# Kernel tuning notes

Hardware: AMD Instinct MI355X
Metric: run time of the kernel (lower is better)

## Reference

```python
import jax, jax.numpy as jnp
import numpy as np

NN_SIZE = 10  # k nearest neighbors (includes the point itself)
EPS = 1e-8


def batch_normals(points_nchw, nn_size):
    # points_nchw: (B, 3, N)
    x = jnp.transpose(points_nchw, (0, 2, 1))  # (B, N, 3)
    sq = jnp.sum(x * x, axis=-1)  # (B, N)
    # pairwise squared distances (B, N, N)
    d2 = sq[:, :, None] + sq[:, None, :] - 2.0 * jnp.einsum('bnd,bmd->bnm', x, x)
    _, idx = jax.lax.top_k(-d2, nn_size)  # (B, N, k) nearest-neighbor indices
    # irregular gather of neighborhoods: (B, N, k, 3)
    neigh = jax.vmap(lambda p, i: p[i])(x, idx)
    centered = neigh - jnp.mean(neigh, axis=2, keepdims=True)
    # local 3x3 covariance per point
    cov = jnp.einsum('bnki,bnkj->bnij', centered, centered) / nn_size
    _, vecs = jnp.linalg.eigh(cov)  # eigenvalues ascending
    normals = vecs[..., 0]  # eigenvector of smallest eigenvalue, (B, N, 3), unit norm
    return jnp.transpose(normals, (0, 2, 1))  # (B, 3, N)


def setup_inputs() -> dict:
    key = jax.random.key(0)
    k1, k2 = jax.random.split(key)
    pred = jax.random.normal(k1, (8, 3, 4096), dtype=jnp.float32)
    gt = jax.random.normal(k2, (8, 3, 4096), dtype=jnp.float32)
    return {"pred": pred, "gt": gt}


def reference(pred, gt):
    pn = batch_normals(pred, NN_SIZE)  # (B, 3, N)
    gn = batch_normals(gt, NN_SIZE)    # (B, 3, N)
    # cosine similarity along the channel (coordinate) dim
    dot = jnp.sum(pn * gn, axis=1)
    denom = jnp.sqrt(jnp.sum(pn * pn, axis=1)) * jnp.sqrt(jnp.sum(gn * gn, axis=1))
    cos = dot / jnp.maximum(denom, EPS)
    return jnp.mean(1.0 - jnp.abs(cos))
```

## Files before the change

### kernel.cpp

```cpp
#include <hip/hip_runtime.h>
#include <float.h>
#include <math.h>

#define BATCH 8
#define NPTS 4096
#define KNN 10
#define BN (BATCH * NPTS)
#define QPB 64
#define SEGS 4
#define HALF (NPTS / 2)
#define SEGC (HALF / SEGS)

__device__ inline float med3f(float x, float a, float b) {
    return __builtin_amdgcn_fmed3f(x, a, b);
}

__device__ inline void smallest_eigvec(float a00, float a01, float a02,
                                       float a11, float a12, float a22,
                                       float& vx, float& vy, float& vz) {
    float p1 = a01 * a01 + a02 * a02 + a12 * a12;
    float q = (a00 + a11 + a22) * (1.0f / 3.0f);
    float b00 = a00 - q, b11 = a11 - q, b22 = a22 - q;
    float p2 = b00 * b00 + b11 * b11 + b22 * b22 + 2.0f * p1;
    float p = sqrtf(p2 * (1.0f / 6.0f));
    if (p < 1e-20f) { vx = 1.0f; vy = 0.0f; vz = 0.0f; return; }
    float ip = 1.0f / p;
    float c00 = b00 * ip, c01 = a01 * ip, c02 = a02 * ip;
    float c11 = b11 * ip, c12 = a12 * ip, c22 = b22 * ip;
    float detB = c00 * (c11 * c22 - c12 * c12)
               - c01 * (c01 * c22 - c12 * c02)
               + c02 * (c01 * c12 - c11 * c02);
    float r = 0.5f * detB;
    r = fminf(1.0f, fmaxf(-1.0f, r));
    float phi = acosf(r) * (1.0f / 3.0f);
    float lmin = q + 2.0f * p * cosf(phi + 2.0943951023931953f);

    float m00 = a00 - lmin, m11 = a11 - lmin, m22 = a22 - lmin;
    float r0x = m00, r0y = a01, r0z = a02;
    float r1x = a01, r1y = m11, r1z = a12;
    float r2x = a02, r2y = a12, r2z = m22;
    float c0x = r0y * r1z - r0z * r1y, c0y = r0z * r1x - r0x * r1z, c0z = r0x * r1y - r0y * r1x;
    float c1x = r0y * r2z - r0z * r2y, c1y = r0z * r2x - r0x * r2z, c1z = r0x * r2y - r0y * r2x;
    float c2x = r1y * r2z - r1z * r2y, c2y = r1z * r2x - r1x * r2z, c2z = r1x * r2y - r1y * r2x;
    float n0 = c0x * c0x + c0y * c0y + c0z * c0z;
    float n1 = c1x * c1x + c1y * c1y + c1z * c1z;
    float n2 = c2x * c2x + c2y * c2y + c2z * c2z;
    float bx = c0x, by = c0y, bz = c0z, bnm = n0;
    if (n1 > bnm) { bx = c1x; by = c1y; bz = c1z; bnm = n1; }
    if (n2 > bnm) { bx = c2x; by = c2y; bz = c2z; bnm = n2; }
    if (bnm < 1e-30f) { vx = 1.0f; vy = 0.0f; vz = 0.0f; return; }
    float inv = rsqrtf(bnm);
    vx = bx * inv; vy = by * inv; vz = bz * inv;
}

__global__ __launch_bounds__(256, 4) void knn_normals_kernel(
    const float* __restrict__ pred, const float* __restrict__ gt,
    float* __restrict__ normals ) {
    __shared__ float4 pts[HALF];
    __shared__ float keybuf[3 * QPB * KNN];

    const int b = blockIdx.y;
    const int cloud = blockIdx.z;
    const float* __restrict__ base = (cloud == 0 ? pred : gt) + b * 3 * NPTS;
    const int tid = threadIdx.x;
    const int q = tid & (QPB - 1);
    const int seg = tid >> 6;
    const int pt = blockIdx.x * QPB + q;

    const float mex = base[pt];
    const float mey = base[NPTS + pt];
    const float mez = base[2 * NPTS + pt];
    const float nmx = -2.0f * mex, nmy = -2.0f * mey, nmz = -2.0f * mez;
    const float smw = mex * mex + mey * mey + mez * mez;

    float k[KNN];
#pragma unroll
    for (int j = 0; j < KNN; ++j) k[j] = FLT_MAX;

    for (int pass = 0; pass < 2; ++pass) {
        const int pb = pass * HALF;
        for (int i = tid; i < HALF; i += 256) {
            float x = base[pb + i];
            float y = base[NPTS + pb + i];
            float z = base[2 * NPTS + pb + i];
            pts[i] = make_float4(x, y, z, x * x + y * y + z * z);
        }
        __syncthreads();

        const int s0 = seg * SEGC;
        const unsigned gbase = (unsigned)(pb + s0);
#pragma unroll 8
        for (int c = 0; c < SEGC; ++c) {
            float4 p = pts[s0 + c];
            float d = fmaf(p.z, nmz, fmaf(p.y, nmy, fmaf(p.x, nmx, p.w + smw)));
            d = fmaxf(d, 1e-30f);
            float key = __uint_as_float((__float_as_uint(d) & 0xFFFFF000u) | (gbase + c));
#pragma unroll
            for (int j = KNN - 1; j >= 1; --j) k[j] = med3f(key, k[j - 1], k[j]);
            k[0] = fminf(key, k[0]);
        }
        __syncthreads();
    }

    if (seg != 0) {
#pragma unroll
        for (int j = 0; j < KNN; ++j) keybuf[((seg - 1) * QPB + q) * KNN + j] = k[j];
    }
    __syncthreads();

    if (seg == 0) {
        for (int s = 0; s < 3; ++s) {
#pragma unroll
            for (int jj = 0; jj < KNN; ++jj) {
                float key = keybuf[(s * QPB + q) * KNN + jj];
#pragma unroll
                for (int j = KNN - 1; j >= 1; --j) k[j] = med3f(key, k[j - 1], k[j]);
                k[0] = fminf(key, k[0]);
            }
        }

        float nx[KNN], ny[KNN], nz[KNN];
        float mx = 0.f, my = 0.f, mz = 0.f;
#pragma unroll
        for (int j = 0; j < KNN; ++j) {
            int idx = (int)(__float_as_uint(k[j]) & 0xFFFu);
            nx[j] = base[idx]; ny[j] = base[NPTS + idx]; nz[j] = base[2 * NPTS + idx];
            mx += nx[j]; my += ny[j]; mz += nz[j];
        }
        mx *= (1.0f / KNN); my *= (1.0f / KNN); mz *= (1.0f / KNN);

        float cxx = 0.f, cxy = 0.f, cxz = 0.f, cyy = 0.f, cyz = 0.f, czz = 0.f;
#pragma unroll
        for (int j = 0; j < KNN; ++j) {
            float dx = nx[j] - mx, dy = ny[j] - my, dz = nz[j] - mz;
            cxx += dx * dx; cxy += dx * dy; cxz += dx * dz;
            cyy += dy * dy; cyz += dy * dz; czz += dz * dz;
        }
        cxx *= (1.0f / KNN); cxy *= (1.0f / KNN); cxz *= (1.0f / KNN);
        cyy *= (1.0f / KNN); cyz *= (1.0f / KNN); czz *= (1.0f / KNN);

        float vx, vy, vz;
        smallest_eigvec(cxx, cxy, cxz, cyy, cyz, czz, vx, vy, vz);

        float* outp = normals + cloud * 3 * BN;
        const int oidx = b * NPTS + pt;
        outp[oidx] = vx;
        outp[BN + oidx] = vy;
        outp[2 * BN + oidx] = vz;
    }
}

__global__ void zero_out_kernel(float* __restrict__ out) {
    if (threadIdx.x == 0) out[0] = 0.0f;
}

__global__ __launch_bounds__(256) void loss_kernel(const float* __restrict__ normals,
                                                   float* __restrict__ out) {
    __shared__ float red[256];
    const float* pn = normals;
    const float* gn = normals + 3 * BN;
    float acc = 0.f;
    for (int i = blockIdx.x * 256 + threadIdx.x; i < BN; i += 64 * 256) {
        float px = pn[i], py = pn[BN + i], pz = pn[2 * BN + i];
        float gx = gn[i], gy = gn[BN + i], gz = gn[2 * BN + i];
        float dot = px * gx + py * gy + pz * gz;
        float npn = sqrtf(px * px + py * py + pz * pz);
        float ngn = sqrtf(gx * gx + gy * gy + gz * gz);
        float denom = fmaxf(npn * ngn, 1e-8f);
        acc += 1.0f - fabsf(dot / denom);
    }
    red[threadIdx.x] = acc;
    __syncthreads();
    for (int s = 128; s > 0; s >>= 1) {
        if (threadIdx.x < s) red[threadIdx.x] += red[threadIdx.x + s];
        __syncthreads();
    }
    if (threadIdx.x == 0) atomicAdd(out, red[0] * (1.0f / BN));
}

extern "C" void kernel_launch(void* const* d_in, const int* in_sizes, int n_in,
                              void* d_out, int out_size, void* d_ws, size_t ws_size,
                              hipStream_t stream) {
    const float* pred = (const float*)d_in[0];
    const float* gt = (const float*)d_in[1];
    float* out = (float*)d_out;
    float* normals = (float*)d_ws;

    dim3 grid(NPTS / QPB, BATCH, 2);
    knn_normals_kernel<<<grid, 256, 0, stream>>>(pred, gt, normals);
    zero_out_kernel<<<1, 64, 0, stream>>>(out);
    loss_kernel<<<64, 256, 0, stream>>>(normals, out);
}
```

Before: 180.2 us.

## Fuse loss into kNN kernel, halve queries per block, quarter staging

Each block now handles 32 query points with 8 candidate segments and stages the cloud in quarters, which halves the shared-memory footprint and allows more resident blocks. The loss reduction moves into the kNN kernel through a last-block atomic counter, which removes the separate zero and loss launches. The covariance is computed from raw sums (E[xx]-mean^2), and the constant |q|^2 term plus the positivity clamp are dropped from the distance key. Risks: the fused reduction runs serially in a single block over 32K points, the raw-sum covariance can lose precision, and negative distance keys can break the float-as-int ordering trick.

Result: slower. 283.1 us (+57.1%).

```diff
diff --git a/kernel.cpp b/kernel.cpp
--- a/kernel.cpp
+++ b/kernel.cpp
@@ -6,10 +6,12 @@
 #define NPTS 4096
 #define KNN 10
 #define BN (BATCH * NPTS)
-#define QPB 64
-#define SEGS 4
-#define HALF (NPTS / 2)
-#define SEGC (HALF / SEGS)
+#define QPB 32
+#define SEGS 8
+#define QUARTER 1024
+#define SEGC (QUARTER / SEGS)
+#define GRIDX (NPTS / QPB)
+#define TOTAL_BLOCKS (GRIDX * BATCH * 2)
 
 __device__ inline float med3f(float x, float a, float b) {
     return __builtin_amdgcn_fmed3f(x, a, b);
@@ -53,48 +55,53 @@
     vx = bx * inv; vy = by * inv; vz = bz * inv;
 }
 
-__global__ __launch_bounds__(256, 4) void knn_normals_kernel(
+__global__ void init_counter_kernel(unsigned* __restrict__ counter) {
+    if (threadIdx.x == 0) *counter = 0u;
+}
+
+__global__ __launch_bounds__(256, 8) void knn_normals_fused(
     const float* __restrict__ pred, const float* __restrict__ gt,
-    float* __restrict__ normals ) {
-    __shared__ float4 pts[HALF];
-    __shared__ float keybuf[3 * QPB * KNN];
+    float* __restrict__ normals , unsigned* __restrict__ counter,
+    float* __restrict__ out) {
+    __shared__ float4 pts[QUARTER];
+    __shared__ float red[256];
+    __shared__ int islast;
 
     const int b = blockIdx.y;
     const int cloud = blockIdx.z;
     const float* __restrict__ base = (cloud == 0 ? pred : gt) + b * 3 * NPTS;
     const int tid = threadIdx.x;
-    const int q = tid & (QPB - 1);
-    const int seg = tid >> 6;
-    const int pt = blockIdx.x * QPB + q;
+    const int lp = tid & (QPB - 1);
+    const int seg = tid >> 5;
+    const int pt = blockIdx.x * QPB + lp;
 
     const float mex = base[pt];
     const float mey = base[NPTS + pt];
     const float mez = base[2 * NPTS + pt];
     const float nmx = -2.0f * mex, nmy = -2.0f * mey, nmz = -2.0f * mez;
-    const float smw = mex * mex + mey * mey + mez * mez;
 
     float k[KNN];
 #pragma unroll
     for (int j = 0; j < KNN; ++j) k[j] = FLT_MAX;
 
-    for (int pass = 0; pass < 2; ++pass) {
-        const int pb = pass * HALF;
-        for (int i = tid; i < HALF; i += 256) {
+    for (int pass = 0; pass < 4; ++pass) {
+        const int pb = pass * QUARTER;
+#pragma unroll
+        for (int i = tid; i < QUARTER; i += 256) {
             float x = base[pb + i];
             float y = base[NPTS + pb + i];
             float z = base[2 * NPTS + pb + i];
-            pts[i] = make_float4(x, y, z, x * x + y * y + z * z);
+            pts[i] = make_float4(x, y, z, fmaf(x, x, fmaf(y, y, z * z)));
         }
         __syncthreads();
 
         const int s0 = seg * SEGC;
-        const unsigned gbase = (unsigned)(pb + s0);
+        const unsigned gb = (unsigned)(pb + s0);
 #pragma unroll 8
         for (int c = 0; c < SEGC; ++c) {
             float4 p = pts[s0 + c];
-            float d = fmaf(p.z, nmz, fmaf(p.y, nmy, fmaf(p.x, nmx, p.w + smw)));
-            d = fmaxf(d, 1e-30f);
-            float key = __uint_as_float((__float_as_uint(d) & 0xFFFFF000u) | (gbase + c));
+            float d = fmaf(p.z, nmz, fmaf(p.y, nmy, fmaf(p.x, nmx, p.w)));
+            float key = __uint_as_float((__float_as_uint(d) & 0xFFFFF000u) | (gb + c));
 #pragma unroll
             for (int j = KNN - 1; j >= 1; --j) k[j] = med3f(key, k[j - 1], k[j]);
             k[0] = fminf(key, k[0]);
@@ -102,42 +109,38 @@
         __syncthreads();
     }
 
+    float* keybuf = (float*)pts;
     if (seg != 0) {
 #pragma unroll
-        for (int j = 0; j < KNN; ++j) keybuf[((seg - 1) * QPB + q) * KNN + j] = k[j];
+        for (int j = 0; j < KNN; ++j) keybuf[((seg - 1) * QPB + lp) * KNN + j] = k[j];
     }
     __syncthreads();
 
     if (seg == 0) {
-        for (int s = 0; s < 3; ++s) {
+        for (int s = 0; s < SEGS - 1; ++s) {
 #pragma unroll
             for (int jj = 0; jj < KNN; ++jj) {
-                float key = keybuf[(s * QPB + q) * KNN + jj];
+                float key = keybuf[(s * QPB + lp) * KNN + jj];
 #pragma unroll
                 for (int j = KNN - 1; j >= 1; --j) k[j] = med3f(key, k[j - 1], k[j]);
                 k[0] = fminf(key, k[0]);
             }
         }
 
-        float nx[KNN], ny[KNN], nz[KNN];
-        float mx = 0.f, my = 0.f, mz = 0.f;
+        float sx = 0.f, sy = 0.f, sz = 0.f;
+        float sxx = 0.f, sxy = 0.f, sxz = 0.f, syy = 0.f, syz = 0.f, szz = 0.f;
 #pragma unroll
         for (int j = 0; j < KNN; ++j) {
             int idx = (int)(__float_as_uint(k[j]) & 0xFFFu);
-            nx[j] = base[idx]; ny[j] = base[NPTS + idx]; nz[j] = base[2 * NPTS + idx];
-            mx += nx[j]; my += ny[j]; mz += nz[j];
+            float x = base[idx], y = base[NPTS + idx], z = base[2 * NPTS + idx];
+            sx += x; sy += y; sz += z;
+            sxx = fmaf(x, x, sxx); sxy = fmaf(x, y, sxy); sxz = fmaf(x, z, sxz);
+            syy = fmaf(y, y, syy); syz = fmaf(y, z, syz); szz = fmaf(z, z, szz);
         }
-        mx *= (1.0f / KNN); my *= (1.0f / KNN); mz *= (1.0f / KNN);
-
-        float cxx = 0.f, cxy = 0.f, cxz = 0.f, cyy = 0.f, cyz = 0.f, czz = 0.f;
-#pragma unroll
-        for (int j = 0; j < KNN; ++j) {
-            float dx = nx[j] - mx, dy = ny[j] - my, dz = nz[j] - mz;
-            cxx += dx * dx; cxy += dx * dy; cxz += dx * dz;
-            cyy += dy * dy; cyz += dy * dz; czz += dz * dz;
-        }
-        cxx *= (1.0f / KNN); cxy *= (1.0f / KNN); cxz *= (1.0f / KNN);
-        cyy *= (1.0f / KNN); cyz *= (1.0f / KNN); czz *= (1.0f / KNN);
+        const float iK = 1.0f / KNN;
+        float mx = sx * iK, my = sy * iK, mz = sz * iK;
+        float cxx = sxx * iK - mx * mx, cxy = sxy * iK - mx * my, cxz = sxz * iK - mx * mz;
+        float cyy = syy * iK - my * my, cyz = syz * iK - my * mz, czz = szz * iK - mz * mz;
 
         float vx, vy, vz;
         smallest_eigvec(cxx, cxy, cxz, cyy, cyz, czz, vx, vy, vz);
@@ -148,34 +151,37 @@
         outp[BN + oidx] = vy;
         outp[2 * BN + oidx] = vz;
     }
-}
 
-__global__ void zero_out_kernel(float* __restrict__ out) {
-    if (threadIdx.x == 0) out[0] = 0.0f;
-}
+    __threadfence();
+    __syncthreads();
+    if (tid == 0) {
+        unsigned old = atomicAdd(counter, 1u);
+        islast = (old == TOTAL_BLOCKS - 1) ? 1 : 0;
+    }
+    __syncthreads();
 
-__global__ __launch_bounds__(256) void loss_kernel(const float* __restrict__ normals,
-                                                   float* __restrict__ out) {
-    __shared__ float red[256];
-    const float* pn = normals;
-    const float* gn = normals + 3 * BN;
-    float acc = 0.f;
-    for (int i = blockIdx.x * 256 + threadIdx.x; i < BN; i += 64 * 256) {
-        float px = pn[i], py = pn[BN + i], pz = pn[2 * BN + i];
-        float gx = gn[i], gy = gn[BN + i], gz = gn[2 * BN + i];
-        float dot = px * gx + py * gy + pz * gz;
-        float npn = sqrtf(px * px + py * py + pz * pz);
-        float ngn = sqrtf(gx * gx + gy * gy + gz * gz);
-        float denom = fmaxf(npn * ngn, 1e-8f);
-        acc += 1.0f - fabsf(dot / denom);
+    if (islast) {
+        __threadfence();
+        const float* pn = normals;
+        const float* gn = normals + 3 * BN;
+        float acc = 0.f;
+        for (int i = tid; i < BN; i += 256) {
+            float px = pn[i], py = pn[BN + i], pz = pn[2 * BN + i];
+            float gx = gn[i], gy = gn[BN + i], gz = gn[2 * BN + i];
+            float dot = px * gx + py * gy + pz * gz;
+            float npn = sqrtf(px * px + py * py + pz * pz);
+            float ngn = sqrtf(gx * gx + gy * gy + gz * gz);
+            float denom = fmaxf(npn * ngn, 1e-8f);
+            acc += 1.0f - fabsf(dot / denom);
+        }
+        red[tid] = acc;
+        __syncthreads();
+        for (int s = 128; s > 0; s >>= 1) {
+            if (tid < s) red[tid] += red[tid + s];
+            __syncthreads();
+        }
+        if (tid == 0) out[0] = red[0] * (1.0f / BN);
     }
-    red[threadIdx.x] = acc;
-    __syncthreads();
-    for (int s = 128; s > 0; s >>= 1) {
-        if (threadIdx.x < s) red[threadIdx.x] += red[threadIdx.x + s];
-        __syncthreads();
-    }
-    if (threadIdx.x == 0) atomicAdd(out, red[0] * (1.0f / BN));
 }
 
 extern "C" void kernel_launch(void* const* d_in, const int* in_sizes, int n_in,
@@ -184,10 +190,10 @@
     const float* pred = (const float*)d_in[0];
     const float* gt = (const float*)d_in[1];
     float* out = (float*)d_out;
-    float* normals = (float*)d_ws;
+    unsigned* counter = (unsigned*)d_ws;
+    float* normals = (float*)d_ws + 4;
 
-    dim3 grid(NPTS / QPB, BATCH, 2);
-    knn_normals_kernel<<<grid, 256, 0, stream>>>(pred, gt, normals);
-    zero_out_kernel<<<1, 64, 0, stream>>>(out);
-    loss_kernel<<<64, 256, 0, stream>>>(normals, out);
+    init_counter_kernel<<<1, 64, 0, stream>>>(counter);
+    dim3 grid(GRIDX, BATCH, 2);
+    knn_normals_fused<<<grid, 256, 0, stream>>>(pred, gt, normals, counter, out);
 }
```
